# Performance work log

Measured on AMD Instinct MI355X. Metric: run time of the kernel, lower is better.

Reference implementation:

```python
import jax, jax.numpy as jnp
import numpy as np

EPS = 1e-5

def _branch(x, W, b, g, beta):
    # Linear -> LayerNorm -> ReLU
    y = jnp.einsum('bnd,od->bno', x, W) + b
    mu = jnp.mean(y, axis=-1, keepdims=True)
    var = jnp.mean(jnp.square(y - mu), axis=-1, keepdims=True)
    y = (y - mu) / jnp.sqrt(var + EPS) * g + beta
    return jax.nn.relu(y)

def setup_inputs() -> dict:
    key = jax.random.key(0)
    ks = jax.random.split(key, 12)
    B, N, D, C = 8, 2048, 1024, 1024
    H = C // 2
    s = 1.0 / np.sqrt(D)
    inp = {
        'sgm': jax.random.normal(ks[0], (B, N, D), jnp.float32),
        'velo': jax.random.normal(ks[1], (B, N, D), jnp.float32),
        'Wq': jax.random.normal(ks[2], (C, D), jnp.float32) * s,
        'bq': jax.random.normal(ks[3], (C,), jnp.float32) * 0.02,
        'gq': jnp.ones((C,), jnp.float32),
        'betaq': jnp.zeros((C,), jnp.float32),
        'Wk': jax.random.normal(ks[4], (C, D), jnp.float32) * s,
        'bk': jax.random.normal(ks[5], (C,), jnp.float32) * 0.02,
        'gk': jnp.ones((C,), jnp.float32),
        'betak': jnp.zeros((C,), jnp.float32),
        'Wv1': jax.random.normal(ks[6], (H, D), jnp.float32) * s,
        'bv1': jax.random.normal(ks[7], (H,), jnp.float32) * 0.02,
        'gv1': jnp.ones((H,), jnp.float32),
        'betav1': jnp.zeros((H,), jnp.float32),
        'Wv2': jax.random.normal(ks[8], (H, D), jnp.float32) * s,
        'bv2': jax.random.normal(ks[9], (H,), jnp.float32) * 0.02,
        'gv2': jnp.ones((H,), jnp.float32),
        'betav2': jnp.zeros((H,), jnp.float32),
    }
    return inp

def reference(sgm, velo, Wq, bq, gq, betaq, Wk, bk, gk, betak,
              Wv1, bv1, gv1, betav1, Wv2, bv2, gv2, betav2):
    q = _branch(sgm, Wq, bq, gq, betaq)      # [B, N, C]
    k = _branch(velo, Wk, bk, gk, betak)     # [B, M, C]
    attn = jnp.einsum('bnc,bmc->bnm', q, k)  # unscaled scores
    attn = jax.nn.softmax(attn, axis=2)
    v1 = _branch(velo, Wv1, bv1, gv1, betav1)  # [B, M, C//2]
    attn = jnp.einsum('bnm,bmh->bnh', attn, v1)
    v2 = _branch(sgm, Wv2, bv2, gv2, betav2)   # [B, N, C//2]
    return jnp.concatenate((v2, attn), axis=2)
```

## Files before the change

### kernel.cpp

```cpp
#include <hip/hip_runtime.h>
#include <hip/hip_bf16.h>


#define BB 8
#define NN 2048
#define DD 1024
#define CC_ 1024
#define HH 512
#define RR (BB*NN)

typedef unsigned short ush;
typedef short bf16x8 __attribute__((ext_vector_type(8)));
typedef float f32x4  __attribute__((ext_vector_type(4)));

#define MiB (1024L*1024L)

__device__ __forceinline__ ush f2bf_rne(float x) {
    unsigned u = __float_as_uint(x);
    return (ush)((u + 0x7fffu + ((u >> 16) & 1u)) >> 16);
}
__device__ __forceinline__ float bf2f(ush h) {
    return __uint_as_float((unsigned)h << 16);
}
__device__ __forceinline__ float wave_sum(float v) {
    #pragma unroll
    for (int o = 32; o; o >>= 1) v += __shfl_down(v, o);
    return v;
}
__device__ __forceinline__ float wave_max(float v) {
    #pragma unroll
    for (int o = 32; o; o >>= 1) v = fmaxf(v, __shfl_down(v, o));
    return v;
}

__device__ __forceinline__ int swzb(int row, int kbyte) {
    return ((row << 6) | kbyte) ^ (((row >> 1) & 3) << 4);
}

__device__ __forceinline__ void glds16(const void* g, void* l) {
    __builtin_amdgcn_global_load_lds(
        (const __attribute__((address_space(1))) unsigned*)g,
        (__attribute__((address_space(3))) unsigned*)l, 16, 0, 0);
}

__global__ __launch_bounds__(512, 2)
void gemm8p_kernel(const ush* __restrict__ Ah, const ush* __restrict__ Al,
                   const ush* __restrict__ Bh, const ush* __restrict__ Bl,
                   float* __restrict__ C, int ldc)
{
    __shared__ ush L[65536];
    constexpr int NT = 48;

    int nwg = gridDim.x * gridDim.y;
    int wg  = blockIdx.x + gridDim.x * blockIdx.y;
    int sz  = (wg & 7) * (nwg >> 3) + (wg >> 3);
    int bx  = sz % gridDim.x, by = sz / gridDim.x;
    const long brow = (long)by << 8, bcol = (long)bx << 8;

    const int t = threadIdx.x, wid = t >> 6, lane = t & 63;
    const int wr = (wid >> 2) << 7;
    const int wc = (wid & 3) << 6;
    const int fr = lane & 15, kg = lane >> 4;

    const int srow = ((wid >> 1) << 4) + (lane >> 2);
    const int scol = ((wid & 1) << 5) + ((((lane & 3) << 3)) ^ ((lane >> 5) << 4));
    const int sdst = wid << 9;

    const int cterm = (fr << 5) + ((kg << 3) ^ ((fr >> 3) << 4));
    const int ha13  = (wr >> 7) << 13;
    const int bbase = 16384 + ((wc >> 7) << 13);
    const int sb0   = (wc & 64) >> 4;

    f32x4 acc[8][4] = {};
    bf16x8 bfrag[4][2];

    auto stage = [&](int X, int half) {
        if (X >= NT) return;
        int pI = X >> 4, kc = (X & 15) << 6;
        const ush* s; long rb;
        if (half < 2) { s = (pI == 1) ? Al : Ah; rb = brow + ((long)(half & 1) << 7); }
        else          { s = (pI == 2) ? Bl : Bh; rb = bcol + ((long)(half & 1) << 7); }
        int lb = ((X & 1) << 15) + ((half >> 1) << 14) + ((half & 1) << 13) + sdst;
        glds16(s + (rb + srow) * 1024 + kc + scol,      &L[lb]);
        glds16(s + (rb + srow + 64) * 1024 + kc + scol, &L[lb + 4096]);
    };

    stage(0, 0); stage(0, 1); stage(0, 2); stage(0, 3);
    stage(1, 2); stage(1, 3);
    asm volatile("s_waitcnt vmcnt(4)");
    __builtin_amdgcn_sched_barrier(0);
    __builtin_amdgcn_s_barrier();

    for (int kt = 0; kt < NT; ++kt) {
        const int ab = (kt & 1) << 15;
        #pragma unroll
        for (int p = 0; p < 4; ++p) {
            bf16x8 afrag[2][2];
            #pragma unroll
            for (int ii = 0; ii < 2; ++ii)
                #pragma unroll
                for (int ks = 0; ks < 2; ++ks)
                    afrag[ii][ks] = *(const bf16x8*)&L[ab + ha13 +
                        ((((2 * p + ii) << 1) | ks) << 9) + cterm];
            if (p == 0) {
                #pragma unroll
                for (int fj = 0; fj < 4; ++fj)
                    #pragma unroll
                    for (int ks = 0; ks < 2; ++ks)
                        bfrag[fj][ks] = *(const bf16x8*)&L[ab + bbase +
                            ((((sb0 + fj) << 1) | ks) << 9) + cterm];
            }
            if      (p == 0) stage(kt + 1, 0);
            else if (p == 1) stage(kt + 1, 1);
            else if (p == 2) stage(kt + 2, 2);
            else             stage(kt + 2, 3);

            __builtin_amdgcn_s_barrier();
            asm volatile("s_waitcnt lgkmcnt(0)");
            __builtin_amdgcn_sched_barrier(0);
            __builtin_amdgcn_s_setprio(1);
            #pragma unroll
            for (int ii = 0; ii < 2; ++ii)
                #pragma unroll
                for (int fj = 0; fj < 4; ++fj)
                    #pragma unroll
                    for (int ks = 0; ks < 2; ++ks)
                        acc[2 * p + ii][fj] = __builtin_amdgcn_mfma_f32_16x16x32_bf16(
                            afrag[ii][ks], bfrag[fj][ks], acc[2 * p + ii][fj], 0, 0, 0);
            __builtin_amdgcn_s_setprio(0);
            if (p == 3) {
                if (kt < NT - 2) asm volatile("s_waitcnt vmcnt(4)");
                else             asm volatile("s_waitcnt vmcnt(0)");
                __builtin_amdgcn_sched_barrier(0);
            }
            __builtin_amdgcn_s_barrier();
        }
    }

    #pragma unroll
    for (int fi = 0; fi < 8; ++fi)
        #pragma unroll
        for (int q = 0; q < 4; ++q) {
            long grow = brow + wr + fi * 16 + (kg << 2) + q;
            float* cr = C + grow * (long)ldc + bcol + wc + fr;
            #pragma unroll
            for (int fj = 0; fj < 4; ++fj) cr[fj << 4] = acc[fi][fj][q];
        }
}

template<int EPI>
__global__ __launch_bounds__(512, 2)
void gemm8q_kernel(const ush* __restrict__ Ah, const ush* __restrict__ Al,
                   const ush* __restrict__ Bh, const ush* __restrict__ Bl,
                   float* __restrict__ C, ush* __restrict__ Pout,
                   float* __restrict__ ml)
{
    __shared__ ush L[49152];
    constexpr int NT = 48;

    long nwg = (long)gridDim.x * gridDim.y * gridDim.z;
    long wg  = (long)blockIdx.x + gridDim.x * ((long)blockIdx.y + (long)gridDim.y * blockIdx.z);
    long sz  = (wg & 7) * (nwg >> 3) + (wg >> 3);
    const int bx = (int)(sz % gridDim.x);
    long rem = sz / gridDim.x;
    const int by = (int)(rem % gridDim.y);
    const long bz = rem / gridDim.y;

    const long brow = (long)by << 8;
    const long bcol = (long)bx << 7;

    const int t = threadIdx.x, wid = t >> 6, lane = t & 63;
    const int wr4 = wid >> 1;
    const int wc2 = wid & 1;
    const int fr = lane & 15, kg = lane >> 4;

    const int srow = ((wid >> 1) << 4) + (lane >> 2);
    const int scol = ((wid & 1) << 5) + (((lane & 3) << 3) ^ ((lane >> 5) << 4));
    const int sdst = wid << 9;

    const int cterm = (fr << 5) + ((kg << 3) ^ ((fr >> 3) << 4));

    const ush* qh = Ah + bz * 2048L * 1024;
    const ush* ql = Al + bz * 2048L * 1024;
    const ush* kh = Bh + bz * 2048L * 1024;
    const ush* kl = Bl + bz * 2048L * 1024;

    f32x4 acc[4][4] = {};
    bf16x8 bfrag[4][2];

    auto stageA = [&](int X, int c) {
        if (X >= NT) return;
        int pI = X >> 4, kc = (X & 15) << 6;
        const ush* s = (pI == 1) ? ql : qh;
        glds16(s + (brow + c * 64 + srow) * 1024 + kc + scol,
               &L[((X & 1) ? 24576 : 0) + ((c * 8) << 9) + sdst]);
    };
    auto stageB = [&](int X, int c) {
        if (X >= NT) return;
        int pI = X >> 4, kc = (X & 15) << 6;
        const ush* s = (pI == 2) ? kl : kh;
        glds16(s + (bcol + c * 64 + srow) * 1024 + kc + scol,
               &L[((X & 1) ? 24576 : 0) + 16384 + ((c * 8) << 9) + sdst]);
    };

    stageA(0, 0); stageA(0, 1); stageA(0, 2); stageA(0, 3);
    stageB(0, 0); stageB(0, 1);
    stageB(1, 0); stageB(1, 1);
    asm volatile("s_waitcnt vmcnt(2)");
    __builtin_amdgcn_sched_barrier(0);
    __builtin_amdgcn_s_barrier();

    for (int kt = 0; kt < NT; ++kt) {
        const int ab = (kt & 1) ? 24576 : 0;
        #pragma unroll
        for (int p = 0; p < 2; ++p) {
            bf16x8 afrag[2][2];
            #pragma unroll
            for (int ii = 0; ii < 2; ++ii)
                #pragma unroll
                for (int ks = 0; ks < 2; ++ks) {
                    int fi = 2 * p + ii;
                    int sA = (wr4 * 4 + fi) * 2 + ks;
                    afrag[ii][ks] = *(const bf16x8*)&L[ab + (sA << 9) + cterm];
                }
            if (p == 0) {
                #pragma unroll
                for (int fj = 0; fj < 4; ++fj)
                    #pragma unroll
                    for (int ks = 0; ks < 2; ++ks) {
                        int sB = (wc2 * 4 + fj) * 2 + ks;
                        bfrag[fj][ks] = *(const bf16x8*)&L[ab + 16384 + (sB << 9) + cterm];
                    }
                stageA(kt + 1, 0); stageA(kt + 1, 1); stageA(kt + 1, 2);
            } else {
                stageA(kt + 1, 3); stageB(kt + 2, 0); stageB(kt + 2, 1);
            }

            __builtin_amdgcn_s_barrier();
            asm volatile("s_waitcnt lgkmcnt(0)");
            __builtin_amdgcn_sched_barrier(0);
            __builtin_amdgcn_s_setprio(1);
            #pragma unroll
            for (int ii = 0; ii < 2; ++ii)
                #pragma unroll
                for (int fj = 0; fj < 4; ++fj)
                    #pragma unroll
                    for (int ks = 0; ks < 2; ++ks)
                        acc[2 * p + ii][fj] = __builtin_amdgcn_mfma_f32_16x16x32_bf16(
                            afrag[ii][ks], bfrag[fj][ks], acc[2 * p + ii][fj], 0, 0, 0);
            __builtin_amdgcn_s_setprio(0);
            if (p == 1) {
                if (kt < NT - 2) asm volatile("s_waitcnt vmcnt(2)");
                else             asm volatile("s_waitcnt vmcnt(0)");
                __builtin_amdgcn_sched_barrier(0);
            }
            __builtin_amdgcn_s_barrier();
        }
    }

    if constexpr (EPI == 1) {
        ush*   Pb  = Pout + bz * 2048L * 512;
        float* mlb = ml + bz * 2048L * 1024;
        #pragma unroll
        for (int fi = 0; fi < 4; ++fi) {
            #pragma unroll
            for (int q = 0; q < 4; ++q) {
                long grow = brow + wr4 * 64 + fi * 16 + (kg << 2) + q;
                float m = mlb[grow * 1024];
                float rs = 0.f;
                #pragma unroll
                for (int fj = 0; fj < 4; ++fj) {
                    float pv = __expf(acc[fi][fj][q] - m);
                    rs += pv;
                    Pb[grow * 512 + bcol + wc2 * 64 + fj * 16 + fr] = f2bf_rne(pv);
                }
                rs += __shfl_xor(rs, 1); rs += __shfl_xor(rs, 2);
                rs += __shfl_xor(rs, 4); rs += __shfl_xor(rs, 8);
                if (fr == 0) atomicAdd(&mlb[grow * 1024 + 1], rs);
            }
        }
    } else {
        float* Cb = C + bz * 2048L * 1024;
        #pragma unroll
        for (int fi = 0; fi < 4; ++fi)
            #pragma unroll
            for (int q = 0; q < 4; ++q) {
                long grow = brow + wr4 * 64 + fi * 16 + (kg << 2) + q;
                float* cr = Cb + grow * 1024 + bcol + wc2 * 64 + fr;
                #pragma unroll
                for (int fj = 0; fj < 4; ++fj) cr[fj << 4] = acc[fi][fj][q];
            }
    }
}

template<int AM, int EPI>
__global__ __launch_bounds__(256, 4)
void gemm3_kernel(const ush* __restrict__ A0, const ush* __restrict__ A1,
                  const ush* __restrict__ B0, const ush* __restrict__ B1,
                  float* __restrict__ C, ush* __restrict__ Pout,
                  float* __restrict__ ml,
                  int K, int lda, int ldb, int ldc,
                  long sAz, long sBz, long sCz, long sPz)
{
    __shared__ alignas(16) ush aHi[128*32];
    __shared__ alignas(16) ush aLo[128*32];
    __shared__ alignas(16) ush bHi[128*32];
    __shared__ alignas(16) ush bLo[128*32];

    long wg  = (long)blockIdx.x +
               (long)gridDim.x * ((long)blockIdx.y + (long)gridDim.y * blockIdx.z);
    long nwg = (long)gridDim.x * gridDim.y * gridDim.z;
    long swz = (wg & 7) * (nwg >> 3) + (wg >> 3);
    const int bx = (int)(swz % gridDim.x);
    long rem = swz / gridDim.x;
    const int by = (int)(rem % gridDim.y);
    const long bz = rem / gridDim.y;

    const long mbase = (long)by << 7;
    const long nbase = (long)bx << 7;
    const int  t    = threadIdx.x;
    const int  wave = t >> 6, lane = t & 63;
    const int  wr = (wave >> 1) << 6;
    const int  wc = (wave & 1)  << 6;
    const int  fr = lane & 15;
    const int  kg = lane >> 4;

    const ush* Ah = A0 + bz * sAz;
    const ush* Bh = B0 + bz * sBz;
    const ush* Bl = B1 + bz * sBz;

    f32x4 acc[4][4] = {};

    for (int k0 = 0; k0 < K; k0 += 32) {
        #pragma unroll
        for (int i = 0; i < 2; ++i) {
            int rl = (wave << 5) + (i << 4) + (lane >> 2);
            int cs = ((lane & 3) ^ ((rl >> 1) & 3)) << 3;
            long goA = (mbase + rl) * (long)lda + k0 + cs;
            long goB = (nbase + rl) * (long)ldb + k0 + cs;
            glds16(Ah + goA, &aHi[(wave << 10) + (i << 9)]);
            if constexpr (AM == 1) {
                const ush* Al_ = A1 + bz * sAz;
                glds16(Al_ + goA, &aLo[(wave << 10) + (i << 9)]);
            }
            glds16(Bh + goB, &bHi[(wave << 10) + (i << 9)]);
            glds16(Bl + goB, &bLo[(wave << 10) + (i << 9)]);
        }
        __syncthreads();

        bf16x8 ah[4], al[4], bh[4], bl[4];
        #pragma unroll
        for (int i = 0; i < 4; ++i) {
            int ra = wr + (i << 4) + fr, rb = wc + (i << 4) + fr;
            ah[i] = *(const bf16x8*)(aHi + (swzb(ra, kg << 4) >> 1));
            if constexpr (AM == 1)
                al[i] = *(const bf16x8*)(aLo + (swzb(ra, kg << 4) >> 1));
            bh[i] = *(const bf16x8*)(bHi + (swzb(rb, kg << 4) >> 1));
            bl[i] = *(const bf16x8*)(bLo + (swzb(rb, kg << 4) >> 1));
        }
        #pragma unroll
        for (int i = 0; i < 4; ++i) {
            #pragma unroll
            for (int j = 0; j < 4; ++j) {
                acc[i][j] = __builtin_amdgcn_mfma_f32_16x16x32_bf16(ah[i], bh[j], acc[i][j], 0, 0, 0);
                acc[i][j] = __builtin_amdgcn_mfma_f32_16x16x32_bf16(ah[i], bl[j], acc[i][j], 0, 0, 0);
                if constexpr (AM == 1)
                    acc[i][j] = __builtin_amdgcn_mfma_f32_16x16x32_bf16(al[i], bh[j], acc[i][j], 0, 0, 0);
            }
        }
        __syncthreads();
    }

    if constexpr (EPI == 1) {
        ush*   Pb  = Pout + bz * sPz;
        float* mlb = ml + bz * 2048L * 1024;
        #pragma unroll
        for (int i = 0; i < 4; ++i) {
            #pragma unroll
            for (int q = 0; q < 4; ++q) {
                long grow = mbase + wr + (i << 4) + (kg << 2) + q;
                float m = mlb[grow * 1024];
                float rs = 0.f;
                #pragma unroll
                for (int j = 0; j < 4; ++j) {
                    float p = __expf(acc[i][j][q] - m);
                    rs += p;
                    Pb[grow * 512 + nbase + wc + (j << 4) + fr] = f2bf_rne(p);
                }
                rs += __shfl_xor(rs, 1); rs += __shfl_xor(rs, 2);
                rs += __shfl_xor(rs, 4); rs += __shfl_xor(rs, 8);
                if (fr == 0) atomicAdd(&mlb[grow * 1024 + 1], rs);
            }
        }
    } else {
        float* Cb = C + bz * sCz;
        #pragma unroll
        for (int i = 0; i < 4; ++i) {
            #pragma unroll
            for (int q = 0; q < 4; ++q) {
                long grow = mbase + wr + (i << 4) + (kg << 2) + q;
                float scale = 1.0f;
                if constexpr (EPI == 3)
                    scale = 1.0f / (ml + bz * 2048L * 1024)[grow * 1024 + 1];
                float* crow = Cb + grow * (long)ldc + nbase + wc + fr;
                #pragma unroll
                for (int j = 0; j < 4; ++j) {
                    if constexpr (EPI == 2)      crow[j << 4] = crow[j << 4] + acc[i][j][q];
                    else if constexpr (EPI == 3) crow[j << 4] = (crow[j << 4] + acc[i][j][q]) * scale;
                    else                         crow[j << 4] = acc[i][j][q];
                }
            }
        }
    }
}

template<int NC, bool HILO>
__global__ void ln_relu_kernel(const float* __restrict__ Y, int ldy,
                               const float* __restrict__ bias,
                               const float* __restrict__ g, const float* __restrict__ beta,
                               float* __restrict__ outf, ush* __restrict__ oh,
                               ush* __restrict__ ol, int ldo)
{
    constexpr int PER = NC / 256;
    long row = blockIdx.x;
    const float* yr = Y + row * (long)ldy;
    int t = threadIdx.x;
    float v[PER]; float s = 0.f, s2 = 0.f;
    #pragma unroll
    for (int i = 0; i < PER; ++i) {
        int c = t + (i << 8);
        float x = yr[c] + bias[c];
        v[i] = x; s += x; s2 += x * x;
    }
    s = wave_sum(s); s2 = wave_sum(s2);
    __shared__ float ra[4], rb[4];
    int w = t >> 6, l = t & 63;
    if (!l) { ra[w] = s; rb[w] = s2; }
    __syncthreads();
    s  = ra[0] + ra[1] + ra[2] + ra[3];
    s2 = rb[0] + rb[1] + rb[2] + rb[3];
    float mu  = s * (1.0f / NC);
    float var = s2 * (1.0f / NC) - mu * mu;
    float inv = rsqrtf(var + 1e-5f);
    #pragma unroll
    for (int i = 0; i < PER; ++i) {
        int c = t + (i << 8);
        float x = (v[i] - mu) * inv * g[c] + beta[c];
        x = fmaxf(x, 0.0f);
        if constexpr (HILO) {
            ush h = f2bf_rne(x);
            ush lo = f2bf_rne(x - __uint_as_float((unsigned)h << 16));
            oh[row * (long)ldo + c] = h;
            ol[row * (long)ldo + c] = lo;
        } else {
            outf[row * (long)ldo + c] = x;
        }
    }
}

__global__ void split_kernel(const float* __restrict__ in, ush* __restrict__ h,
                             ush* __restrict__ l, long n)
{
    long i = ((long)blockIdx.x * 256 + threadIdx.x) * 4;
    if (i >= n) return;
    float4 v = *(const float4*)(in + i);
    ushort4 hh, ll;
    hh.x = f2bf_rne(v.x); ll.x = f2bf_rne(v.x - __uint_as_float((unsigned)hh.x << 16));
    hh.y = f2bf_rne(v.y); ll.y = f2bf_rne(v.y - __uint_as_float((unsigned)hh.y << 16));
    hh.z = f2bf_rne(v.z); ll.z = f2bf_rne(v.z - __uint_as_float((unsigned)hh.z << 16));
    hh.w = f2bf_rne(v.w); ll.w = f2bf_rne(v.w - __uint_as_float((unsigned)hh.w << 16));
    *(ushort4*)(h + i) = hh;
    *(ushort4*)(l + i) = ll;
}

__global__ void transpose_split_kernel(const float* __restrict__ in,
                                       ush* __restrict__ oh, ush* __restrict__ ol)
{
    __shared__ float tile[32][33];
    long bz = blockIdx.z;
    const float* I = in + bz * (long)NN * HH;
    ush* OH = oh + bz * (long)HH * NN;
    ush* OL = ol + bz * (long)HH * NN;
    int c0 = blockIdx.x << 5, r0 = blockIdx.y << 5;
    int tx = threadIdx.x & 31, ty = threadIdx.x >> 5;
    #pragma unroll
    for (int i = 0; i < 32; i += 8)
        tile[ty + i][tx] = I[(long)(r0 + ty + i) * HH + c0 + tx];
    __syncthreads();
    #pragma unroll
    for (int i = 0; i < 32; i += 8) {
        float x = tile[tx][ty + i];
        ush h = f2bf_rne(x);
        ush lo = f2bf_rne(x - __uint_as_float((unsigned)h << 16));
        long o = (long)(c0 + ty + i) * NN + r0 + tx;
        OH[o] = h; OL[o] = lo;
    }
}

__global__ void exp_pass_kernel(float* __restrict__ ml, ush* __restrict__ P)
{
    long row = blockIdx.x;
    float* sr = ml + row * 1024;
    int t = threadIdx.x;
    float s0 = sr[t], s1 = sr[t + 256];
    float m = fmaxf(s0, s1);
    m = wave_max(m);
    __shared__ float ra[4], rb[4];
    int w = t >> 6, l = t & 63;
    if (!l) ra[w] = m;
    __syncthreads();
    m = fmaxf(fmaxf(ra[0], ra[1]), fmaxf(ra[2], ra[3]));
    float p0 = __expf(s0 - m), p1 = __expf(s1 - m);
    ush h0 = f2bf_rne(p0), h1 = f2bf_rne(p1);
    P[row * 512 + t] = h0;
    P[row * 512 + t + 256] = h1;
    float ls = bf2f(h0) + bf2f(h1);
    ls = wave_sum(ls);
    if (!l) rb[w] = ls;
    __syncthreads();
    if (t == 0) {
        sr[0] = m;
        sr[1] = rb[0] + rb[1] + rb[2] + rb[3];
    }
}

extern "C" void kernel_launch(void* const* d_in, const int* in_sizes, int n_in,
                              void* d_out, int out_size, void* d_ws, size_t ws_size,
                              hipStream_t stream)
{
    const float* sgm   = (const float*)d_in[0];
    const float* velo  = (const float*)d_in[1];
    const float* Wq    = (const float*)d_in[2];
    const float* bq    = (const float*)d_in[3];
    const float* gq    = (const float*)d_in[4];
    const float* betaq = (const float*)d_in[5];
    const float* Wk    = (const float*)d_in[6];
    const float* bk    = (const float*)d_in[7];
    const float* gk    = (const float*)d_in[8];
    const float* betak = (const float*)d_in[9];
    const float* Wv1   = (const float*)d_in[10];
    const float* bv1   = (const float*)d_in[11];
    const float* gv1   = (const float*)d_in[12];
    const float* betav1= (const float*)d_in[13];
    const float* Wv2   = (const float*)d_in[14];
    const float* bv2   = (const float*)d_in[15];
    const float* gv2   = (const float*)d_in[16];
    const float* betav2= (const float*)d_in[17];
    float* out = (float*)d_out;
    char*  wsb = (char*)d_ws;

    if (ws_size < 176 * MiB) return;

    ush* xh   = (ush*)wsb;
    ush* xl   = (ush*)(wsb + 32 * MiB);
    ush* kh   = (ush*)(wsb + 64 * MiB);
    ush* kl   = (ush*)(wsb + 96 * MiB);
    ush* v1th = (ush*)(wsb + 128 * MiB);
    ush* v1tl = (ush*)(wsb + 144 * MiB);
    ush* Wqh  = (ush*)(wsb + 160 * MiB);
    ush* Wql  = (ush*)(wsb + 162 * MiB);
    ush* Wkh  = (ush*)(wsb + 164 * MiB);
    ush* Wkl  = (ush*)(wsb + 166 * MiB);
    ush* Wv1h = (ush*)(wsb + 168 * MiB);
    ush* Wv1l = (ush*)(wsb + 169 * MiB);
    ush* P    = (ush*)(wsb + 160 * MiB);
    float* v1f = out + 8388608L;

    dim3 blk(256);

    split_kernel<<<1024, blk, 0, stream>>>(Wq,  Wqh,  Wql,  (long)CC_*DD);
    split_kernel<<<1024, blk, 0, stream>>>(Wk,  Wkh,  Wkl,  (long)CC_*DD);
    split_kernel<<<512,  blk, 0, stream>>>(Wv1, Wv1h, Wv1l, (long)HH*DD);

    split_kernel<<<16384, blk, 0, stream>>>(velo, xh, xl, (long)RR*DD);
    gemm8p_kernel<<<dim3(4, 64), dim3(512), 0, stream>>>(xh, xl, Wkh, Wkl, out, CC_);
    ln_relu_kernel<1024,true><<<RR, blk, 0, stream>>>(out, CC_, bk, gk, betak, nullptr, kh, kl, CC_);
    gemm3_kernel<1,0><<<dim3(4,128,1), blk, 0, stream>>>(
        xh, xl, Wv1h, Wv1l, out, nullptr, nullptr, DD, DD, DD, HH, 0, 0, 0, 0);
    ln_relu_kernel<512,false><<<RR, blk, 0, stream>>>(out, HH, bv1, gv1, betav1, v1f, nullptr, nullptr, HH);
    transpose_split_kernel<<<dim3(16,64,BB), blk, 0, stream>>>(v1f, v1th, v1tl);

    split_kernel<<<16384, blk, 0, stream>>>(sgm, xh, xl, (long)RR*DD);
    gemm8p_kernel<<<dim3(4, 64), dim3(512), 0, stream>>>(xh, xl, Wqh, Wql, out, CC_);
    ln_relu_kernel<1024,true><<<RR, blk, 0, stream>>>(out, CC_, bq, gq, betaq, nullptr, xh, xl, CC_);

    gemm8q_kernel<0><<<dim3(4, 8, 8), dim3(512), 0, stream>>>(
        xh, xl, kh, kl, out, nullptr, nullptr);
    exp_pass_kernel<<<RR, blk, 0, stream>>>(out, P);
    gemm3_kernel<2,0><<<dim3(4,16,8), blk, 0, stream>>>(
        P, nullptr, v1th, v1tl, out + HH, nullptr, nullptr,
        512, 512, NN, CC_, 2048L*512, 512L*2048, 2048L*1024, 0);
    for (int s = 1; s < 4; ++s) {
        gemm8q_kernel<1><<<dim3(4, 8, 8), dim3(512), 0, stream>>>(
            xh, xl, kh + (long)s*512*1024, kl + (long)s*512*1024,
            nullptr, P, out);
        if (s < 3)
            gemm3_kernel<2,2><<<dim3(4,16,8), blk, 0, stream>>>(
                P, nullptr, v1th + s*512, v1tl + s*512,
                out + HH, nullptr, nullptr, 512, 512, NN, CC_,
                2048L*512, 512L*2048, 2048L*1024, 0);
        else
            gemm3_kernel<2,3><<<dim3(4,16,8), blk, 0, stream>>>(
                P, nullptr, v1th + s*512, v1tl + s*512,
                out + HH, nullptr, out, 512, 512, NN, CC_,
                2048L*512, 512L*2048, 2048L*1024, 0);
    }

    split_kernel<<<16384, blk, 0, stream>>>(sgm, xh, xl, (long)RR*DD);
    ush* Wv2h = (ush*)(wsb + 160 * MiB);
    ush* Wv2l = (ush*)(wsb + 161 * MiB);
    split_kernel<<<512, blk, 0, stream>>>(Wv2, Wv2h, Wv2l, (long)HH*DD);
    gemm3_kernel<1,0><<<dim3(4,128,1), blk, 0, stream>>>(
        xh, xl, Wv2h, Wv2l, out, nullptr, nullptr, DD, DD, DD, CC_, 0, 0, 0, 0);
    ln_relu_kernel<512,false><<<RR, blk, 0, stream>>>(out, CC_, bv2, gv2, betav2, out, nullptr, nullptr, CC_);
}
```

Before: 840.6 us.

## Drop low-order split for V1 in PV GEMM and route V GEMMs through 8-wave kernel

```diff
diff --git a/kernel.cpp b/kernel.cpp
--- a/kernel.cpp
+++ b/kernel.cpp
@@ -153,7 +153,7 @@
 void gemm8q_kernel(const ush* __restrict__ Ah, const ush* __restrict__ Al,
                    const ush* __restrict__ Bh, const ush* __restrict__ Bl,
                    float* __restrict__ C, ush* __restrict__ Pout,
-                   float* __restrict__ ml)
+                   float* __restrict__ ml, int ldc)
 {
     __shared__ ush L[49152];
     constexpr int NT = 48;
@@ -286,7 +286,7 @@
             #pragma unroll
             for (int q = 0; q < 4; ++q) {
                 long grow = brow + wr4 * 64 + fi * 16 + (kg << 2) + q;
-                float* cr = Cb + grow * 1024 + bcol + wc2 * 64 + fr;
+                float* cr = Cb + grow * (long)ldc + bcol + wc2 * 64 + fr;
                 #pragma unroll
                 for (int fj = 0; fj < 4; ++fj) cr[fj << 4] = acc[fi][fj][q];
             }
@@ -327,7 +327,6 @@
 
     const ush* Ah = A0 + bz * sAz;
     const ush* Bh = B0 + bz * sBz;
-    const ush* Bl = B1 + bz * sBz;
 
     f32x4 acc[4][4] = {};
 
@@ -344,7 +343,10 @@
                 glds16(Al_ + goA, &aLo[(wave << 10) + (i << 9)]);
             }
             glds16(Bh + goB, &bHi[(wave << 10) + (i << 9)]);
-            glds16(Bl + goB, &bLo[(wave << 10) + (i << 9)]);
+            if constexpr (AM != 3) {
+                const ush* Bl_ = B1 + bz * sBz;
+                glds16(Bl_ + goB, &bLo[(wave << 10) + (i << 9)]);
+            }
         }
         __syncthreads();
 
@@ -356,14 +358,16 @@
             if constexpr (AM == 1)
                 al[i] = *(const bf16x8*)(aLo + (swzb(ra, kg << 4) >> 1));
             bh[i] = *(const bf16x8*)(bHi + (swzb(rb, kg << 4) >> 1));
-            bl[i] = *(const bf16x8*)(bLo + (swzb(rb, kg << 4) >> 1));
+            if constexpr (AM != 3)
+                bl[i] = *(const bf16x8*)(bLo + (swzb(rb, kg << 4) >> 1));
         }
         #pragma unroll
         for (int i = 0; i < 4; ++i) {
             #pragma unroll
             for (int j = 0; j < 4; ++j) {
                 acc[i][j] = __builtin_amdgcn_mfma_f32_16x16x32_bf16(ah[i], bh[j], acc[i][j], 0, 0, 0);
-                acc[i][j] = __builtin_amdgcn_mfma_f32_16x16x32_bf16(ah[i], bl[j], acc[i][j], 0, 0, 0);
+                if constexpr (AM != 3)
+                    acc[i][j] = __builtin_amdgcn_mfma_f32_16x16x32_bf16(ah[i], bl[j], acc[i][j], 0, 0, 0);
                 if constexpr (AM == 1)
                     acc[i][j] = __builtin_amdgcn_mfma_f32_16x16x32_bf16(al[i], bh[j], acc[i][j], 0, 0, 0);
             }
@@ -371,28 +375,7 @@
         __syncthreads();
     }
 
-    if constexpr (EPI == 1) {
-        ush*   Pb  = Pout + bz * sPz;
-        float* mlb = ml + bz * 2048L * 1024;
-        #pragma unroll
-        for (int i = 0; i < 4; ++i) {
-            #pragma unroll
-            for (int q = 0; q < 4; ++q) {
-                long grow = mbase + wr + (i << 4) + (kg << 2) + q;
-                float m = mlb[grow * 1024];
-                float rs = 0.f;
-                #pragma unroll
-                for (int j = 0; j < 4; ++j) {
-                    float p = __expf(acc[i][j][q] - m);
-                    rs += p;
-                    Pb[grow * 512 + nbase + wc + (j << 4) + fr] = f2bf_rne(p);
-                }
-                rs += __shfl_xor(rs, 1); rs += __shfl_xor(rs, 2);
-                rs += __shfl_xor(rs, 4); rs += __shfl_xor(rs, 8);
-                if (fr == 0) atomicAdd(&mlb[grow * 1024 + 1], rs);
-            }
-        }
-    } else {
+    {
         float* Cb = C + bz * sCz;
         #pragma unroll
         for (int i = 0; i < 4; ++i) {
@@ -474,13 +457,12 @@
 }
 
 __global__ void transpose_split_kernel(const float* __restrict__ in,
-                                       ush* __restrict__ oh, ush* __restrict__ ol)
+                                       ush* __restrict__ oh)
 {
     __shared__ float tile[32][33];
     long bz = blockIdx.z;
     const float* I = in + bz * (long)NN * HH;
     ush* OH = oh + bz * (long)HH * NN;
-    ush* OL = ol + bz * (long)HH * NN;
     int c0 = blockIdx.x << 5, r0 = blockIdx.y << 5;
     int tx = threadIdx.x & 31, ty = threadIdx.x >> 5;
     #pragma unroll
@@ -490,10 +472,8 @@
     #pragma unroll
     for (int i = 0; i < 32; i += 8) {
         float x = tile[tx][ty + i];
-        ush h = f2bf_rne(x);
-        ush lo = f2bf_rne(x - __uint_as_float((unsigned)h << 16));
         long o = (long)(c0 + ty + i) * NN + r0 + tx;
-        OH[o] = h; OL[o] = lo;
+        OH[o] = f2bf_rne(x);
     }
 }
 
@@ -556,7 +536,6 @@
     ush* kh   = (ush*)(wsb + 64 * MiB);
     ush* kl   = (ush*)(wsb + 96 * MiB);
     ush* v1th = (ush*)(wsb + 128 * MiB);
-    ush* v1tl = (ush*)(wsb + 144 * MiB);
     ush* Wqh  = (ush*)(wsb + 160 * MiB);
     ush* Wql  = (ush*)(wsb + 162 * MiB);
     ush* Wkh  = (ush*)(wsb + 164 * MiB);
@@ -575,33 +554,33 @@
     split_kernel<<<16384, blk, 0, stream>>>(velo, xh, xl, (long)RR*DD);
     gemm8p_kernel<<<dim3(4, 64), dim3(512), 0, stream>>>(xh, xl, Wkh, Wkl, out, CC_);
     ln_relu_kernel<1024,true><<<RR, blk, 0, stream>>>(out, CC_, bk, gk, betak, nullptr, kh, kl, CC_);
-    gemm3_kernel<1,0><<<dim3(4,128,1), blk, 0, stream>>>(
-        xh, xl, Wv1h, Wv1l, out, nullptr, nullptr, DD, DD, DD, HH, 0, 0, 0, 0);
+    gemm8q_kernel<0><<<dim3(4, 64, 1), dim3(512), 0, stream>>>(
+        xh, xl, Wv1h, Wv1l, out, nullptr, nullptr, HH);
     ln_relu_kernel<512,false><<<RR, blk, 0, stream>>>(out, HH, bv1, gv1, betav1, v1f, nullptr, nullptr, HH);
-    transpose_split_kernel<<<dim3(16,64,BB), blk, 0, stream>>>(v1f, v1th, v1tl);
+    transpose_split_kernel<<<dim3(16,64,BB), blk, 0, stream>>>(v1f, v1th);
 
     split_kernel<<<16384, blk, 0, stream>>>(sgm, xh, xl, (long)RR*DD);
     gemm8p_kernel<<<dim3(4, 64), dim3(512), 0, stream>>>(xh, xl, Wqh, Wql, out, CC_);
     ln_relu_kernel<1024,true><<<RR, blk, 0, stream>>>(out, CC_, bq, gq, betaq, nullptr, xh, xl, CC_);
 
     gemm8q_kernel<0><<<dim3(4, 8, 8), dim3(512), 0, stream>>>(
-        xh, xl, kh, kl, out, nullptr, nullptr);
+        xh, xl, kh, kl, out, nullptr, nullptr, 1024);
     exp_pass_kernel<<<RR, blk, 0, stream>>>(out, P);
-    gemm3_kernel<2,0><<<dim3(4,16,8), blk, 0, stream>>>(
-        P, nullptr, v1th, v1tl, out + HH, nullptr, nullptr,
+    gemm3_kernel<3,0><<<dim3(4,16,8), blk, 0, stream>>>(
+        P, nullptr, v1th, nullptr, out + HH, nullptr, nullptr,
         512, 512, NN, CC_, 2048L*512, 512L*2048, 2048L*1024, 0);
     for (int s = 1; s < 4; ++s) {
         gemm8q_kernel<1><<<dim3(4, 8, 8), dim3(512), 0, stream>>>(
             xh, xl, kh + (long)s*512*1024, kl + (long)s*512*1024,
-            nullptr, P, out);
+            nullptr, P, out, 0);
         if (s < 3)
-            gemm3_kernel<2,2><<<dim3(4,16,8), blk, 0, stream>>>(
-                P, nullptr, v1th + s*512, v1tl + s*512,
+            gemm3_kernel<3,2><<<dim3(4,16,8), blk, 0, stream>>>(
+                P, nullptr, v1th + s*512, nullptr,
                 out + HH, nullptr, nullptr, 512, 512, NN, CC_,
                 2048L*512, 512L*2048, 2048L*1024, 0);
         else
-            gemm3_kernel<2,3><<<dim3(4,16,8), blk, 0, stream>>>(
-                P, nullptr, v1th + s*512, v1tl + s*512,
+            gemm3_kernel<3,3><<<dim3(4,16,8), blk, 0, stream>>>(
+                P, nullptr, v1th + s*512, nullptr,
                 out + HH, nullptr, out, 512, 512, NN, CC_,
                 2048L*512, 512L*2048, 2048L*1024, 0);
     }
@@ -610,7 +589,7 @@
     ush* Wv2h = (ush*)(wsb + 160 * MiB);
     ush* Wv2l = (ush*)(wsb + 161 * MiB);
     split_kernel<<<512, blk, 0, stream>>>(Wv2, Wv2h, Wv2l, (long)HH*DD);
-    gemm3_kernel<1,0><<<dim3(4,128,1), blk, 0, stream>>>(
-        xh, xl, Wv2h, Wv2l, out, nullptr, nullptr, DD, DD, DD, CC_, 0, 0, 0, 0);
+    gemm8q_kernel<0><<<dim3(4, 64, 1), dim3(512), 0, stream>>>(
+        xh, xl, Wv2h, Wv2l, out, nullptr, nullptr, CC_);
     ln_relu_kernel<512,false><<<RR, blk, 0, stream>>>(out, CC_, bv2, gv2, betav2, out, nullptr, nullptr, CC_);
 }
```

New measurement: 796.9 us. 5.2% less time.
